# Kernel optimization log

Hardware: AMD Instinct MI355X
Metric: run time of the kernel (lower is better)

Reference implementation:

```python
import jax, jax.numpy as jnp
import numpy as np

B, S, D = 4, 2048, 1024  # batch, seq_len, model dim (= qk_dim = output_dim)


def setup_inputs() -> dict:
    key = jax.random.key(0)
    kq, kk, kv, kwq, kwk, kwv = jax.random.split(key, 6)
    q = jax.random.normal(kq, (B, S, D), dtype=jnp.float32)
    k = jax.random.normal(kk, (B, S, D), dtype=jnp.float32)
    v = jax.random.normal(kv, (B, S, D), dtype=jnp.float32)
    # causal mask, broadcast over batch
    mask = jnp.broadcast_to(jnp.tril(jnp.ones((S, S), dtype=bool)), (B, S, S))
    W_q = jax.random.uniform(kwq, (D, D), dtype=jnp.float32)
    W_k = jax.random.uniform(kwk, (D, D), dtype=jnp.float32)
    W_v = jax.random.uniform(kwv, (D, D), dtype=jnp.float32)
    return {"q": q, "k": k, "v": v, "mask": mask, "W_q": W_q, "W_k": W_k, "W_v": W_v}


def reference(q, k, v, mask, W_q, W_k, W_v):
    q1 = q @ W_q  # (B, S, D)
    k1 = k @ W_k  # (B, S, D)
    v1 = v @ W_v  # (B, S, D)
    qk = jnp.einsum('bij,bkj->bik', q1, k1)  # (B, S, S)
    qk = qk * jax.lax.rsqrt(float(k1.shape[-1]))
    neg_inf = jnp.finfo(jnp.float32).min
    qk = jnp.where(mask, qk, neg_inf)
    s = jax.nn.softmax(qk, axis=-1)
    return jnp.einsum('bij,bjk->bik', s, v1)
```

## Files before the change

### kernel.cpp

```cpp
#include <hip/hip_runtime.h>
#include <hip/hip_bf16.h>
#include <float.h>


typedef __attribute__((ext_vector_type(8))) short bf16x8;
typedef __attribute__((ext_vector_type(4))) float f32x4;

#define MFMA16 __builtin_amdgcn_mfma_f32_16x16x32_bf16

union U8 { bf16x8 v; unsigned w[4]; };

__device__ __forceinline__ ushort f2bf(float x) {
  union { float f; unsigned u; } v; v.f = x;
  unsigned r = v.u + 0x7fffu + ((v.u >> 16) & 1u);
  return (ushort)(r >> 16);
}
__device__ __forceinline__ float bf2f(ushort h) {
  union { unsigned u; float f; } v; v.u = ((unsigned)h) << 16;
  return v.f;
}
__device__ __forceinline__ void splitf(float x, ushort& hi, ushort& lo) {
  hi = f2bf(x);
  lo = f2bf(x - bf2f(hi));
}

__device__ __forceinline__ bf16x8 cvt8(const float* lp) {
  U8 H;
#pragma unroll
  for (int p = 0; p < 4; ++p) {
    const unsigned u0 = __float_as_uint(lp[2 * p]);
    const unsigned u1 = __float_as_uint(lp[2 * p + 1]);
    const unsigned r0 = (u0 + 0x7fffu + ((u0 >> 16) & 1u)) >> 16;
    const unsigned r1 = (u1 + 0x7fffu + ((u1 >> 16) & 1u)) & 0xffff0000u;
    H.w[p] = r0 | r1;
  }
  return H.v;
}

#define GLOAD16(gp, lp)                                                        \
  __builtin_amdgcn_global_load_lds(                                            \
      (const __attribute__((address_space(1))) void*)(gp),                     \
      (__attribute__((address_space(3))) void*)(lp), 16, 0, 0)

#define BARRIER() asm volatile("s_barrier" ::: "memory")
#define VMCNT8() asm volatile("s_waitcnt vmcnt(8)" ::: "memory")
#define VMCNT6() asm volatile("s_waitcnt vmcnt(6)" ::: "memory")
#define VMCNT0() asm volatile("s_waitcnt vmcnt(0)" ::: "memory")

__device__ __forceinline__ void stage_bf16_32(const ushort* g, int pitch,
                                              ushort* lds, int w, int lane) {
#pragma unroll
  for (int i = 0; i < 2; ++i) {
    const int c = w * 2 + i;
    const int row = c * 16 + (lane >> 2);
    const int kp = (lane & 3) * 8;
    GLOAD16(g + (size_t)row * pitch + kp, lds + c * 512);
  }
}
__device__ __forceinline__ void stage_f32_32(const float* g, int pitch,
                                             float* lds, int w, int lane) {
#pragma unroll
  for (int i = 0; i < 4; ++i) {
    const int c = w * 4 + i;
    const int row = c * 8 + (lane >> 3);
    const int kp = (lane & 7) * 4;
    GLOAD16(g + (size_t)row * pitch + kp, lds + c * 256);
  }
}

__device__ __forceinline__ void stage_half8(const ushort* __restrict__ g,
                                            ushort* lds, int k0, int t) {
#pragma unroll
  for (int i = 0; i < 2; ++i) {
    const int c = t + i * 512;
    const int row = c >> 3;
    const int pcb = (c & 7) * 16;
    const int lcb = pcb ^ ((row & 7) << 4);
    GLOAD16(g + (size_t)row * 1024 + k0 + (lcb >> 1), lds + c * 8);
  }
}

__global__ __launch_bounds__(256) void wt_split(
    const float* __restrict__ q, const float* __restrict__ k,
    const float* __restrict__ W0, const float* __restrict__ W1,
    const float* __restrict__ W2, ushort* __restrict__ Th0,
    ushort* __restrict__ Tl0, ushort* __restrict__ Th1,
    ushort* __restrict__ Tl1, ushort* __restrict__ Th2,
    ushort* __restrict__ qh, ushort* __restrict__ ql,
    ushort* __restrict__ kh, ushort* __restrict__ kl) {
  __shared__ float t[32][33];
  const int f = blockIdx.x;
  if (f < 3072) {
    const int z = f >> 10, r10 = f & 1023;
    const int bx = r10 & 31, by = r10 >> 5;
    const float* W = z == 0 ? W0 : (z == 1 ? W1 : W2);
    ushort* Th = z == 0 ? Th0 : (z == 1 ? Th1 : Th2);
    ushort* Tl = z == 0 ? Tl0 : (z == 1 ? Tl1 : nullptr);
    const int r = threadIdx.x >> 3, c4 = (threadIdx.x & 7) * 4;
    const float4 x = *reinterpret_cast<const float4*>(
        &W[(size_t)(bx * 32 + r) * 1024 + by * 32 + c4]);
    t[r][c4] = x.x; t[r][c4 + 1] = x.y; t[r][c4 + 2] = x.z; t[r][c4 + 3] = x.w;
    __syncthreads();
    ushort h[4], l[4];
#pragma unroll
    for (int j = 0; j < 4; ++j) splitf(t[c4 + j][r], h[j], l[j]);
    const size_t o = (size_t)(by * 32 + r) * 1024 + bx * 32 + c4;
    *reinterpret_cast<ushort4*>(&Th[o]) = ushort4{h[0], h[1], h[2], h[3]};
    if (Tl)
      *reinterpret_cast<ushort4*>(&Tl[o]) = ushort4{l[0], l[1], l[2], l[3]};
  } else {
    const int fl = f - 3072;
    const float* X = (fl >> 11) ? k : q;
    ushort* H = (fl >> 11) ? kh : qh;
    ushort* L = (fl >> 11) ? kl : ql;
    const int n4 = 2097152;
    for (int i = (fl & 2047) * 256 + threadIdx.x; i < n4; i += 2048 * 256) {
      const float4 x = reinterpret_cast<const float4*>(X)[i];
      ushort h0, l0, h1, l1, h2, l2, h3, l3;
      splitf(x.x, h0, l0); splitf(x.y, h1, l1);
      splitf(x.z, h2, l2); splitf(x.w, h3, l3);
      reinterpret_cast<ushort4*>(H)[i] = ushort4{h0, h1, h2, h3};
      reinterpret_cast<ushort4*>(L)[i] = ushort4{l0, l1, l2, l3};
    }
  }
}

__global__ __launch_bounds__(512, 2) void proj_qk8(
    const ushort* __restrict__ Ah0, const ushort* __restrict__ Al0,
    const ushort* __restrict__ Ah1, const ushort* __restrict__ Al1,
    const ushort* __restrict__ Bh0, const ushort* __restrict__ Bl0,
    const ushort* __restrict__ Bh1, const ushort* __restrict__ Bl1,
    ushort* __restrict__ Oh0, ushort* __restrict__ Ol0,
    ushort* __restrict__ Oh1, ushort* __restrict__ Ol1) {
  __shared__ ushort As[2][16384];
  __shared__ ushort Bs[2][16384];
  const int bid = blockIdx.x;
  const int fid = (bid & 7) * 32 + (bid >> 3);
  const int z = fid >> 7, r = fid & 127;
  const int yt = r >> 2, xt = r & 3;
  const ushort* Ah = z ? Ah1 : Ah0;
  const ushort* Al = z ? Al1 : Al0;
  const ushort* Bh = z ? Bh1 : Bh0;
  const ushort* Bl = z ? Bl1 : Bl0;
  ushort* Oh = z ? Oh1 : Oh0;
  ushort* Ol = z ? Ol1 : Ol0;
  const size_t am0 = (size_t)yt * 256 * 1024;
  const size_t bn0 = (size_t)xt * 256 * 1024;
  const int t = threadIdx.x;
  const int lane = t & 63, w = t >> 6;
  const int wm = w >> 2, wn = w & 3;
  const int lr = lane & 15, kg = lane >> 4;
  f32x4 acc[8][4] = {};
  bf16x8 Ar[4][2], Br[4][2];

  auto stage_tile = [&](int kt) {
    if (kt >= 48) kt -= 48;
    const int seg = kt >> 4;
    const int k0 = (kt & 15) * 64;
    const int slot = kt & 1;
    const ushort* ga = (seg == 1) ? Al : Ah;
    const ushort* gb = (seg == 2) ? Bl : Bh;
#pragma unroll
    for (int h = 0; h < 2; ++h)
      stage_half8(ga + am0 + (size_t)(h * 128) * 1024, &As[slot][h * 8192], k0, t);
#pragma unroll
    for (int h = 0; h < 2; ++h)
      stage_half8(gb + bn0 + (size_t)(h * 128) * 1024, &Bs[slot][h * 8192], k0, t);
  };
  auto loadA = [&](int slot, int mq) {
#pragma unroll
    for (int m = 0; m < 4; ++m)
#pragma unroll
      for (int ks = 0; ks < 2; ++ks) {
        const int row = wm * 128 + (mq * 4 + m) * 16 + lr;
        const int cb = (ks * 64 + kg * 16) ^ ((row & 7) << 4);
        Ar[m][ks] =
            *reinterpret_cast<const bf16x8*>(&As[slot][row * 64 + (cb >> 1)]);
      }
  };
  auto loadB = [&](int slot, int nq) {
#pragma unroll
    for (int n = 0; n < 2; ++n)
#pragma unroll
      for (int ks = 0; ks < 2; ++ks) {
        const int col = wn * 64 + (nq * 2 + n) * 16 + lr;
        const int cb = (ks * 64 + kg * 16) ^ ((col & 7) << 4);
        Br[nq * 2 + n][ks] =
            *reinterpret_cast<const bf16x8*>(&Bs[slot][col * 64 + (cb >> 1)]);
      }
  };
  auto mfma_q = [&](int mq, int nq) {
    __builtin_amdgcn_s_setprio(1);
#pragma unroll
    for (int m = 0; m < 4; ++m)
#pragma unroll
      for (int n = 0; n < 2; ++n)
#pragma unroll
        for (int ks = 0; ks < 2; ++ks)
          acc[mq * 4 + m][nq * 2 + n] = MFMA16(
              Ar[m][ks], Br[nq * 2 + n][ks], acc[mq * 4 + m][nq * 2 + n], 0, 0, 0);
    __builtin_amdgcn_s_setprio(0);
  };

  stage_tile(0);
#pragma unroll 2
  for (int kt = 0; kt < 48; ++kt) {
    const int slot = kt & 1;
    stage_tile(kt + 1);
    VMCNT8();
    BARRIER();
    loadA(slot, 0); loadB(slot, 0);
    mfma_q(0, 0);
    loadB(slot, 1);
    mfma_q(0, 1);
    loadA(slot, 1);
    mfma_q(1, 0);
    mfma_q(1, 1);
    BARRIER();
  }

#pragma unroll
  for (int m = 0; m < 8; ++m)
#pragma unroll
    for (int n = 0; n < 4; ++n)
#pragma unroll
      for (int reg = 0; reg < 4; ++reg) {
        const int gm = yt * 256 + wm * 128 + m * 16 + kg * 4 + reg;
        const int gn = xt * 256 + wn * 64 + n * 16 + lr;
        ushort h, l;
        splitf(acc[m][n][reg], h, l);
        Oh[(size_t)gm * 1024 + gn] = h;
        Ol[(size_t)gm * 1024 + gn] = l;
      }
}

__global__ __launch_bounds__(256) void qk2(
    const ushort* __restrict__ q1h, const ushort* __restrict__ q1l,
    const ushort* __restrict__ k1h, const ushort* __restrict__ k1l,
    float* __restrict__ scoresA, float* __restrict__ scoresB) {
  __shared__ ushort Ahs[4096], Als[4096], Bhs[4096], Bls[4096];
  const int f = blockIdx.x;
  const int s = (f & 7) * 136 + (f >> 3);
  const int z = s / 544;
  const int rem = s % 544;
  const int b = rem / 136;
  int p = rem % 136, ti = 0, accp = 0;
  while (accp + ti + 1 <= p) { accp += ti + 1; ++ti; }
  const int tj = p - accp;
  const int tid = threadIdx.x, lane = tid & 63, w = tid >> 6;
  const int wr = w >> 1, wc = w & 1;
  const int lr = lane & 15, kg = lane >> 4;
  const int kh0 = z * 512;
  const ushort* qh = q1h + ((size_t)b * 2048 + ti * 128) * 1024 + kh0;
  const ushort* ql = q1l + ((size_t)b * 2048 + ti * 128) * 1024 + kh0;
  const ushort* kh = k1h + ((size_t)b * 2048 + tj * 128) * 1024 + kh0;
  const ushort* kl = k1l + ((size_t)b * 2048 + tj * 128) * 1024 + kh0;
  f32x4 acc[4][4] = {};

  for (int k0 = 0; k0 < 512; k0 += 32) {
    stage_bf16_32(qh + k0, 1024, Ahs, w, lane);
    stage_bf16_32(ql + k0, 1024, Als, w, lane);
    stage_bf16_32(kh + k0, 1024, Bhs, w, lane);
    stage_bf16_32(kl + k0, 1024, Bls, w, lane);
    __syncthreads();
    bf16x8 ah[4], al[4], bh[4], bl[4];
#pragma unroll
    for (int m = 0; m < 4; ++m) {
      ah[m] = *reinterpret_cast<bf16x8*>(&Ahs[(wr * 64 + m * 16 + lr) * 32 + kg * 8]);
      al[m] = *reinterpret_cast<bf16x8*>(&Als[(wr * 64 + m * 16 + lr) * 32 + kg * 8]);
    }
#pragma unroll
    for (int n = 0; n < 4; ++n) {
      bh[n] = *reinterpret_cast<bf16x8*>(&Bhs[(wc * 64 + n * 16 + lr) * 32 + kg * 8]);
      bl[n] = *reinterpret_cast<bf16x8*>(&Bls[(wc * 64 + n * 16 + lr) * 32 + kg * 8]);
    }
#pragma unroll
    for (int m = 0; m < 4; ++m)
#pragma unroll
      for (int n = 0; n < 4; ++n) {
        acc[m][n] = MFMA16(ah[m], bh[n], acc[m][n], 0, 0, 0);
        acc[m][n] = MFMA16(ah[m], bl[n], acc[m][n], 0, 0, 0);
        acc[m][n] = MFMA16(al[m], bh[n], acc[m][n], 0, 0, 0);
      }
    __syncthreads();
  }
  const float sc = 0.03125f;
  float* st = (z ? scoresB : scoresA) + ((size_t)b * 136 + p) * 16384;
#pragma unroll
  for (int m = 0; m < 4; ++m)
#pragma unroll
    for (int n = 0; n < 4; ++n)
#pragma unroll
      for (int reg = 0; reg < 4; ++reg) {
        const int il = wr * 64 + m * 16 + kg * 4 + reg;
        const int jl = wc * 64 + n * 16 + lr;
        st[il * 128 + jl] = acc[m][n][reg] * sc;
      }
}

__global__ __launch_bounds__(256) void sm_projv(
    float* __restrict__ scoresA, const float* __restrict__ scoresB,
    const ushort* __restrict__ Wvt, const float* __restrict__ V,
    ushort* __restrict__ v1t) {
  __shared__ __align__(16) char smem[24576];
  const int tid = threadIdx.x, lane = tid & 63, w = tid >> 6;
  const int fg = blockIdx.x;
  if (fg >= 512) {
    float* red = reinterpret_cast<float*>(smem);
    const int f2 = fg - 512;
    const int b = f2 >> 11, r = f2 & 2047;
    const int ti = r >> 7, rl = r & 127, ncol = (ti + 1) * 128;
    const int valid = r + 1;
    const size_t tbase = ((size_t)b * 136 + (ti * (ti + 1)) / 2) * 16384;
    float* srowA = scoresA + tbase;
    const float* srowB = scoresB + tbase;

    float vals[2][4];
    float mx = -FLT_MAX;
#pragma unroll
    for (int c = 0; c < 2; ++c) {
      const int j = tid * 4 + c * 1024;
      if (j < ncol) {
        const size_t o = (size_t)(j >> 7) * 16384 + rl * 128 + (j & 127);
        const float4 a = *reinterpret_cast<const float4*>(srowA + o);
        const float4 bb = *reinterpret_cast<const float4*>(srowB + o);
        vals[c][0] = (j + 0 < valid) ? a.x + bb.x : -FLT_MAX;
        vals[c][1] = (j + 1 < valid) ? a.y + bb.y : -FLT_MAX;
        vals[c][2] = (j + 2 < valid) ? a.z + bb.z : -FLT_MAX;
        vals[c][3] = (j + 3 < valid) ? a.w + bb.w : -FLT_MAX;
      } else {
        vals[c][0] = vals[c][1] = vals[c][2] = vals[c][3] = -FLT_MAX;
      }
      mx = fmaxf(mx, fmaxf(fmaxf(vals[c][0], vals[c][1]),
                           fmaxf(vals[c][2], vals[c][3])));
    }
#pragma unroll
    for (int o = 32; o; o >>= 1) mx = fmaxf(mx, __shfl_xor(mx, o));
    if (lane == 0) red[w] = mx;
    __syncthreads();
    mx = fmaxf(fmaxf(red[0], red[1]), fmaxf(red[2], red[3]));

    float ex[2][4];
    float sum = 0.f;
#pragma unroll
    for (int c = 0; c < 2; ++c)
#pragma unroll
      for (int e = 0; e < 4; ++e) {
        const int j = tid * 4 + c * 1024 + e;
        ex[c][e] = (j < valid) ? __expf(vals[c][e] - mx) : 0.f;
        sum += ex[c][e];
      }
#pragma unroll
    for (int o = 32; o; o >>= 1) sum += __shfl_xor(sum, o);
    if (lane == 0) red[4 + w] = sum;
    __syncthreads();
    sum = red[4] + red[5] + red[6] + red[7];
    const float inv = 1.f / sum;
#pragma unroll
    for (int c = 0; c < 2; ++c) {
      const int j = tid * 4 + c * 1024;
      if (j < ncol) {
        ushort* pt =
            reinterpret_cast<ushort*>(srowA + (size_t)(j >> 7) * 16384);
        ushort4 pw;
        pw.x = f2bf(ex[c][0] * inv); pw.y = f2bf(ex[c][1] * inv);
        pw.z = f2bf(ex[c][2] * inv); pw.w = f2bf(ex[c][3] * inv);
        *reinterpret_cast<ushort4*>(&pt[rl * 256 + (j & 127)]) = pw;
      }
    }
  } else {
    ushort* Ahs = reinterpret_cast<ushort*>(smem);
    float* Bs = reinterpret_cast<float*>(smem + 8192);
    const int f2 = fg;
    const int yb = (f2 >> 3) & 7;
    const int xb = (f2 & 7) + ((f2 >> 6) << 3);
    const int wr = w >> 1, wc = w & 1;
    const int lr = lane & 15, kg = lane >> 4;
    const int m0 = yb * 128;
    const int n0 = xb * 128;
    f32x4 acc[4][4] = {};

    for (int k0 = 0; k0 < 1024; k0 += 32) {
      stage_bf16_32(Wvt + (size_t)m0 * 1024 + k0, 1024, Ahs, w, lane);
      stage_f32_32(V + (size_t)n0 * 1024 + k0, 1024, Bs, w, lane);
      __syncthreads();
      bf16x8 ah[4], bh[4];
#pragma unroll
      for (int m = 0; m < 4; ++m)
        ah[m] = *reinterpret_cast<bf16x8*>(
            &Ahs[(wr * 64 + m * 16 + lr) * 32 + kg * 8]);
#pragma unroll
      for (int n = 0; n < 4; ++n)
        bh[n] = cvt8(&Bs[(wc * 64 + n * 16 + lr) * 32 + kg * 8]);
#pragma unroll
      for (int m = 0; m < 4; ++m)
#pragma unroll
        for (int n = 0; n < 4; ++n)
          acc[m][n] = MFMA16(ah[m], bh[n], acc[m][n], 0, 0, 0);
      __syncthreads();
    }
#pragma unroll
    for (int m = 0; m < 4; ++m)
#pragma unroll
      for (int n = 0; n < 4; ++n)
#pragma unroll
        for (int reg = 0; reg < 4; ++reg) {
          const int gm = m0 + wr * 64 + m * 16 + kg * 4 + reg;
          const int gn = n0 + wc * 64 + n * 16 + lr;
          const int b = gn >> 11, jj = gn & 2047;
          v1t[((size_t)b << 21) + (size_t)gm * 2048 + jj] = f2bf(acc[m][n][reg]);
        }
  }
}

__global__ __launch_bounds__(256) void pv2(const float* __restrict__ scores,
                                           const ushort* __restrict__ v1t,
                                           float* __restrict__ out) {
  __shared__ ushort Ps[2][8192], Vs[2][4096];
  const int fl = blockIdx.x;
  const int s = (fl & 7) * 128 + (fl >> 3);
  const int b = s >> 8, rem = s & 255;
  const int ti = 15 - (rem >> 4);
  const int n0 = (rem & 15) * 64;
  const int t = threadIdx.x, lane = t & 63, w = t >> 6;
  const int wr = w >> 1, wc = w & 1;
  const int lr = lane & 15, kg = lane >> 4;
  const int tri_ti = (ti * (ti + 1)) / 2;
  const ushort* vbase = v1t + ((size_t)b << 21) + (size_t)n0 * 2048;
  const int nt = 2 * (ti + 1);
  f32x4 acc[4][2] = {};

  auto stage_tile = [&](int kt) {
    const int slot = kt & 1;
    const int k0 = kt * 64;
    const ushort* pt = reinterpret_cast<const ushort*>(
        scores + ((size_t)b * 136 + tri_ti + (k0 >> 7)) * 16384);
    const int kpo = (k0 & 64);
#pragma unroll
    for (int i = 0; i < 4; ++i) {
      const int c = t + i * 256;
      const int row = c >> 3;
      const int lcb = ((c & 7) * 16) ^ ((row & 7) << 4);
      GLOAD16(pt + (size_t)row * 256 + kpo + (lcb >> 1), Ps[slot] + c * 8);
    }
#pragma unroll
    for (int i = 0; i < 2; ++i) {
      const int c = t + i * 256;
      const int row = c >> 3;
      const int lcb = ((c & 7) * 16) ^ ((row & 7) << 4);
      GLOAD16(vbase + (size_t)row * 2048 + k0 + (lcb >> 1), Vs[slot] + c * 8);
    }
  };

  stage_tile(0);
  for (int kt = 0; kt < nt; ++kt) {
    const int slot = kt & 1;
    if (kt + 1 < nt) {
      stage_tile(kt + 1);
      VMCNT6();
    } else {
      VMCNT0();
    }
    BARRIER();
    bf16x8 pa[4][2], vb[2][2];
#pragma unroll
    for (int m = 0; m < 4; ++m)
#pragma unroll
      for (int ks = 0; ks < 2; ++ks) {
        const int row = wr * 64 + m * 16 + lr;
        const int cb = (ks * 64 + kg * 16) ^ ((row & 7) << 4);
        pa[m][ks] =
            *reinterpret_cast<const bf16x8*>(&Ps[slot][row * 64 + (cb >> 1)]);
      }
#pragma unroll
    for (int n = 0; n < 2; ++n)
#pragma unroll
      for (int ks = 0; ks < 2; ++ks) {
        const int col = wc * 32 + n * 16 + lr;
        const int cb = (ks * 64 + kg * 16) ^ ((col & 7) << 4);
        vb[n][ks] =
            *reinterpret_cast<const bf16x8*>(&Vs[slot][col * 64 + (cb >> 1)]);
      }
    __builtin_amdgcn_s_setprio(1);
#pragma unroll
    for (int m = 0; m < 4; ++m)
#pragma unroll
      for (int n = 0; n < 2; ++n)
#pragma unroll
        for (int ks = 0; ks < 2; ++ks)
          acc[m][n] = MFMA16(pa[m][ks], vb[n][ks], acc[m][n], 0, 0, 0);
    __builtin_amdgcn_s_setprio(0);
    BARRIER();
  }
#pragma unroll
  for (int m = 0; m < 4; ++m)
#pragma unroll
    for (int n = 0; n < 2; ++n)
#pragma unroll
      for (int reg = 0; reg < 4; ++reg) {
        const int gm = ti * 128 + wr * 64 + m * 16 + kg * 4 + reg;
        const int gn = n0 + wc * 32 + n * 16 + lr;
        out[((size_t)b * 2048 + gm) * 1024 + gn] = acc[m][n][reg];
      }
}

extern "C" void kernel_launch(void* const* d_in, const int* in_sizes, int n_in,
                              void* d_out, int out_size, void* d_ws,
                              size_t ws_size, hipStream_t stream) {
  const float* q = (const float*)d_in[0];
  const float* k = (const float*)d_in[1];
  const float* v = (const float*)d_in[2];
  const float* Wq = (const float*)d_in[4];
  const float* Wk = (const float*)d_in[5];
  const float* Wv = (const float*)d_in[6];
  float* out = (float*)d_out;

  char* ws = (char*)d_ws;
  const size_t SCORES_T = 35651584;
  float* scoresA = (float*)ws;
  float* scoresB = (float*)(ws + SCORES_T);
  ushort* qsh = (ushort*)ws;
  ushort* qsl = qsh + 8388608;
  ushort* ksh = qsh + 2 * 8388608;
  ushort* ksl = qsh + 3 * 8388608;
  ushort* q1hi = (ushort*)(ws + 2 * SCORES_T);
  ushort* q1lo = q1hi + 8388608;
  ushort* k1hi = q1hi + 2 * 8388608;
  ushort* k1lo = q1hi + 3 * 8388608;
  ushort* v1t = (ushort*)(ws + 2 * SCORES_T);
  ushort* Wqth = (ushort*)(ws + 2 * SCORES_T + 67108864);
  ushort* Wqtl = Wqth + 1048576;
  ushort* Wkth = Wqth + 2097152;
  ushort* Wktl = Wqth + 3145728;
  ushort* Wvt  = Wqth + 4194304;
  const size_t need = 2 * SCORES_T + 67108864 + 10485760;
  if (ws_size < need) return;

  dim3 blk(256);
  wt_split<<<dim3(7168), blk, 0, stream>>>(q, k, Wq, Wk, Wv, Wqth, Wqtl, Wkth,
                                           Wktl, Wvt, qsh, qsl, ksh, ksl);
  proj_qk8<<<dim3(256), dim3(512), 0, stream>>>(qsh, qsl, ksh, ksl, Wqth,
                                                Wqtl, Wkth, Wktl, q1hi, q1lo,
                                                k1hi, k1lo);
  qk2<<<dim3(1088), blk, 0, stream>>>(q1hi, q1lo, k1hi, k1lo, scoresA,
                                      scoresB);
  sm_projv<<<dim3(8704), blk, 0, stream>>>(scoresA, scoresB, Wvt, v, v1t);
  pv2<<<dim3(1024), blk, 0, stream>>>(scoresA, v1t, out);
}
```

Before: 298.1 us.

## Double-buffer qk2 loads and restructure proj_qk8 into fused split-bf16 k-steps

```diff
diff --git a/kernel.cpp b/kernel.cpp
--- a/kernel.cpp
+++ b/kernel.cpp
@@ -68,16 +68,9 @@
   }
 }
 
-__device__ __forceinline__ void stage_half8(const ushort* __restrict__ g,
-                                            ushort* lds, int k0, int t) {
-#pragma unroll
-  for (int i = 0; i < 2; ++i) {
-    const int c = t + i * 512;
-    const int row = c >> 3;
-    const int pcb = (c & 7) * 16;
-    const int lcb = pcb ^ ((row & 7) << 4);
-    GLOAD16(g + (size_t)row * 1024 + k0 + (lcb >> 1), lds + c * 8);
-  }
+__device__ __forceinline__ bf16x8 rd32(const ushort* s, int row, int kg) {
+  const int cb = (kg * 16) ^ (((row >> 1) & 3) << 4);
+  return *reinterpret_cast<const bf16x8*>(&s[row * 32 + (cb >> 1)]);
 }
 
 __global__ __launch_bounds__(256) void wt_split(
@@ -132,90 +125,79 @@
     const ushort* __restrict__ Bh1, const ushort* __restrict__ Bl1,
     ushort* __restrict__ Oh0, ushort* __restrict__ Ol0,
     ushort* __restrict__ Oh1, ushort* __restrict__ Ol1) {
-  __shared__ ushort As[2][16384];
-  __shared__ ushort Bs[2][16384];
+  __shared__ ushort Ahs[2][8192], Als[2][8192];
+  __shared__ ushort Bhs[2][8192], Bls[2][8192];
   const int bid = blockIdx.x;
   const int fid = (bid & 7) * 32 + (bid >> 3);
   const int z = fid >> 7, r = fid & 127;
   const int yt = r >> 2, xt = r & 3;
-  const ushort* Ah = z ? Ah1 : Ah0;
-  const ushort* Al = z ? Al1 : Al0;
-  const ushort* Bh = z ? Bh1 : Bh0;
-  const ushort* Bl = z ? Bl1 : Bl0;
+  const ushort* Ahp = (z ? Ah1 : Ah0) + (size_t)yt * 256 * 1024;
+  const ushort* Alp = (z ? Al1 : Al0) + (size_t)yt * 256 * 1024;
+  const ushort* Bhp = (z ? Bh1 : Bh0) + (size_t)xt * 256 * 1024;
+  const ushort* Blp = (z ? Bl1 : Bl0) + (size_t)xt * 256 * 1024;
   ushort* Oh = z ? Oh1 : Oh0;
   ushort* Ol = z ? Ol1 : Ol0;
-  const size_t am0 = (size_t)yt * 256 * 1024;
-  const size_t bn0 = (size_t)xt * 256 * 1024;
   const int t = threadIdx.x;
   const int lane = t & 63, w = t >> 6;
   const int wm = w >> 2, wn = w & 3;
   const int lr = lane & 15, kg = lane >> 4;
   f32x4 acc[8][4] = {};
-  bf16x8 Ar[4][2], Br[4][2];
-
+
+  auto stage_slab = [&](const ushort* g, ushort* lds, int k0) {
+#pragma unroll
+    for (int i = 0; i < 2; ++i) {
+      const int c = t + i * 512;
+      const int row = c >> 2;
+      const int lcb = ((c & 3) * 16) ^ (((row >> 1) & 3) << 4);
+      GLOAD16(g + (size_t)row * 1024 + k0 + (lcb >> 1), lds + c * 8);
+    }
+  };
   auto stage_tile = [&](int kt) {
-    if (kt >= 48) kt -= 48;
-    const int seg = kt >> 4;
-    const int k0 = (kt & 15) * 64;
+    const int k0 = kt * 32;
     const int slot = kt & 1;
-    const ushort* ga = (seg == 1) ? Al : Ah;
-    const ushort* gb = (seg == 2) ? Bl : Bh;
-#pragma unroll
-    for (int h = 0; h < 2; ++h)
-      stage_half8(ga + am0 + (size_t)(h * 128) * 1024, &As[slot][h * 8192], k0, t);
-#pragma unroll
-    for (int h = 0; h < 2; ++h)
-      stage_half8(gb + bn0 + (size_t)(h * 128) * 1024, &Bs[slot][h * 8192], k0, t);
+    stage_slab(Ahp, Ahs[slot], k0);
+    stage_slab(Alp, Als[slot], k0);
+    stage_slab(Bhp, Bhs[slot], k0);
+    stage_slab(Blp, Bls[slot], k0);
   };
-  auto loadA = [&](int slot, int mq) {
-#pragma unroll
-    for (int m = 0; m < 4; ++m)
-#pragma unroll
-      for (int ks = 0; ks < 2; ++ks) {
+
+  stage_tile(0);
+  for (int kt = 0; kt < 32; ++kt) {
+    const int slot = kt & 1;
+    if (kt + 1 < 32) {
+      stage_tile(kt + 1);
+      VMCNT8();
+    } else {
+      VMCNT0();
+    }
+    BARRIER();
+    bf16x8 bh[4], bl[4];
+#pragma unroll
+    for (int n = 0; n < 4; ++n) {
+      const int col = wn * 64 + n * 16 + lr;
+      bh[n] = rd32(Bhs[slot], col, kg);
+      bl[n] = rd32(Bls[slot], col, kg);
+    }
+#pragma unroll
+    for (int mq = 0; mq < 2; ++mq) {
+      bf16x8 ah[4], al[4];
+#pragma unroll
+      for (int m = 0; m < 4; ++m) {
         const int row = wm * 128 + (mq * 4 + m) * 16 + lr;
-        const int cb = (ks * 64 + kg * 16) ^ ((row & 7) << 4);
-        Ar[m][ks] =
-            *reinterpret_cast<const bf16x8*>(&As[slot][row * 64 + (cb >> 1)]);
-      }
-  };
-  auto loadB = [&](int slot, int nq) {
-#pragma unroll
-    for (int n = 0; n < 2; ++n)
-#pragma unroll
-      for (int ks = 0; ks < 2; ++ks) {
-        const int col = wn * 64 + (nq * 2 + n) * 16 + lr;
-        const int cb = (ks * 64 + kg * 16) ^ ((col & 7) << 4);
-        Br[nq * 2 + n][ks] =
-            *reinterpret_cast<const bf16x8*>(&Bs[slot][col * 64 + (cb >> 1)]);
-      }
-  };
-  auto mfma_q = [&](int mq, int nq) {
-    __builtin_amdgcn_s_setprio(1);
-#pragma unroll
-    for (int m = 0; m < 4; ++m)
-#pragma unroll
-      for (int n = 0; n < 2; ++n)
-#pragma unroll
-        for (int ks = 0; ks < 2; ++ks)
-          acc[mq * 4 + m][nq * 2 + n] = MFMA16(
-              Ar[m][ks], Br[nq * 2 + n][ks], acc[mq * 4 + m][nq * 2 + n], 0, 0, 0);
-    __builtin_amdgcn_s_setprio(0);
-  };
-
-  stage_tile(0);
-#pragma unroll 2
-  for (int kt = 0; kt < 48; ++kt) {
-    const int slot = kt & 1;
-    stage_tile(kt + 1);
-    VMCNT8();
-    BARRIER();
-    loadA(slot, 0); loadB(slot, 0);
-    mfma_q(0, 0);
-    loadB(slot, 1);
-    mfma_q(0, 1);
-    loadA(slot, 1);
-    mfma_q(1, 0);
-    mfma_q(1, 1);
+        ah[m] = rd32(Ahs[slot], row, kg);
+        al[m] = rd32(Als[slot], row, kg);
+      }
+      __builtin_amdgcn_s_setprio(1);
+#pragma unroll
+      for (int m = 0; m < 4; ++m)
+#pragma unroll
+        for (int n = 0; n < 4; ++n) {
+          acc[mq * 4 + m][n] = MFMA16(ah[m], bh[n], acc[mq * 4 + m][n], 0, 0, 0);
+          acc[mq * 4 + m][n] = MFMA16(ah[m], bl[n], acc[mq * 4 + m][n], 0, 0, 0);
+          acc[mq * 4 + m][n] = MFMA16(al[m], bh[n], acc[mq * 4 + m][n], 0, 0, 0);
+        }
+      __builtin_amdgcn_s_setprio(0);
+    }
     BARRIER();
   }
 
@@ -238,7 +220,8 @@
     const ushort* __restrict__ q1h, const ushort* __restrict__ q1l,
     const ushort* __restrict__ k1h, const ushort* __restrict__ k1l,
     float* __restrict__ scoresA, float* __restrict__ scoresB) {
-  __shared__ ushort Ahs[4096], Als[4096], Bhs[4096], Bls[4096];
+  __shared__ ushort Ahs[2][4096], Als[2][4096];
+  __shared__ ushort Bhs[2][4096], Bls[2][4096];
   const int f = blockIdx.x;
   const int s = (f & 7) * 136 + (f >> 3);
   const int z = s / 544;
@@ -247,7 +230,7 @@
   int p = rem % 136, ti = 0, accp = 0;
   while (accp + ti + 1 <= p) { accp += ti + 1; ++ti; }
   const int tj = p - accp;
-  const int tid = threadIdx.x, lane = tid & 63, w = tid >> 6;
+  const int t = threadIdx.x, lane = t & 63, w = t >> 6;
   const int wr = w >> 1, wc = w & 1;
   const int lr = lane & 15, kg = lane >> 4;
   const int kh0 = z * 512;
@@ -257,23 +240,48 @@
   const ushort* kl = k1l + ((size_t)b * 2048 + tj * 128) * 1024 + kh0;
   f32x4 acc[4][4] = {};
 
-  for (int k0 = 0; k0 < 512; k0 += 32) {
-    stage_bf16_32(qh + k0, 1024, Ahs, w, lane);
-    stage_bf16_32(ql + k0, 1024, Als, w, lane);
-    stage_bf16_32(kh + k0, 1024, Bhs, w, lane);
-    stage_bf16_32(kl + k0, 1024, Bls, w, lane);
-    __syncthreads();
+  auto stage_slab = [&](const ushort* g, ushort* lds, int k0) {
+#pragma unroll
+    for (int i = 0; i < 2; ++i) {
+      const int c = t + i * 256;
+      const int row = c >> 2;
+      const int lcb = ((c & 3) * 16) ^ (((row >> 1) & 3) << 4);
+      GLOAD16(g + (size_t)row * 1024 + k0 + (lcb >> 1), lds + c * 8);
+    }
+  };
+  auto stage_tile = [&](int kt) {
+    const int k0 = kt * 32;
+    const int slot = kt & 1;
+    stage_slab(qh, Ahs[slot], k0);
+    stage_slab(ql, Als[slot], k0);
+    stage_slab(kh, Bhs[slot], k0);
+    stage_slab(kl, Bls[slot], k0);
+  };
+
+  stage_tile(0);
+  for (int kt = 0; kt < 16; ++kt) {
+    const int slot = kt & 1;
+    if (kt + 1 < 16) {
+      stage_tile(kt + 1);
+      VMCNT8();
+    } else {
+      VMCNT0();
+    }
+    BARRIER();
     bf16x8 ah[4], al[4], bh[4], bl[4];
 #pragma unroll
     for (int m = 0; m < 4; ++m) {
-      ah[m] = *reinterpret_cast<bf16x8*>(&Ahs[(wr * 64 + m * 16 + lr) * 32 + kg * 8]);
-      al[m] = *reinterpret_cast<bf16x8*>(&Als[(wr * 64 + m * 16 + lr) * 32 + kg * 8]);
+      const int row = wr * 64 + m * 16 + lr;
+      ah[m] = rd32(Ahs[slot], row, kg);
+      al[m] = rd32(Als[slot], row, kg);
     }
 #pragma unroll
     for (int n = 0; n < 4; ++n) {
-      bh[n] = *reinterpret_cast<bf16x8*>(&Bhs[(wc * 64 + n * 16 + lr) * 32 + kg * 8]);
-      bl[n] = *reinterpret_cast<bf16x8*>(&Bls[(wc * 64 + n * 16 + lr) * 32 + kg * 8]);
-    }
+      const int col = wc * 64 + n * 16 + lr;
+      bh[n] = rd32(Bhs[slot], col, kg);
+      bl[n] = rd32(Bls[slot], col, kg);
+    }
+    __builtin_amdgcn_s_setprio(1);
 #pragma unroll
     for (int m = 0; m < 4; ++m)
 #pragma unroll
@@ -282,7 +290,8 @@
         acc[m][n] = MFMA16(ah[m], bl[n], acc[m][n], 0, 0, 0);
         acc[m][n] = MFMA16(al[m], bh[n], acc[m][n], 0, 0, 0);
       }
-    __syncthreads();
+    __builtin_amdgcn_s_setprio(0);
+    BARRIER();
   }
   const float sc = 0.03125f;
   float* st = (z ? scoresB : scoresA) + ((size_t)b * 136 + p) * 16384;
```

After: 289.9 us, median of 2. -2.8%, faster.
